# Kernel optimization log

Measured on AMD Instinct MI355X. Metric: run time of the kernel, lower is better.

The kernel has to match this reference:

```python
import jax, jax.numpy as jnp
import numpy as np

B, C_IN, C_OUT, H, W, K = 64, 64, 128, 64, 64, 3


def setup_inputs() -> dict:
    key = jax.random.key(0)
    k1, k2, k3 = jax.random.split(key, 3)
    x = jax.random.normal(k1, (B, C_IN, H, W), dtype=jnp.float32)
    weight = jax.random.normal(k2, (C_OUT, C_IN, K, K), dtype=jnp.float32)
    bias = jax.random.normal(k3, (C_OUT, 1, 1), dtype=jnp.float32)
    return {"x": x, "weight": weight, "bias": bias}


def reference(x, weight, bias):
    # Valid (no pad), stride-1, NCHW direct conv + broadcast bias, matching
    # the naive nested-loop conv2d_multi_in_out + bias of MyConv2D.
    out = jax.lax.conv_general_dilated(
        x, weight,
        window_strides=(1, 1),
        padding="VALID",
        dimension_numbers=("NCHW", "OIHW", "NCHW"),
    )
    return out + bias  # bias (C_out,1,1) broadcasts over (B, C_out, H_out, W_out)
```

## Files before the change

kernel.cpp:

```cpp
#include <hip/hip_runtime.h>

#define CI 64
#define CO 128
#define HH 64
#define WW 64
#define OH 62
#define OW 62

typedef __attribute__((ext_vector_type(8))) short short8x;
typedef __attribute__((ext_vector_type(16))) float f32x16;

__device__ ushort g_wt[9 * CO * CI];

__device__ __forceinline__ ushort bf16rne(float f) {
    unsigned u = __builtin_bit_cast(unsigned, f);
    u += 0x7fffu + ((u >> 16) & 1u);
    return (ushort)(u >> 16);
}

__global__ __launch_bounds__(256)
void wprep(const float* __restrict__ w) {
    const int idx = blockIdx.x * 256 + threadIdx.x;
    const int kk = idx >> 13;
    const int rem = idx & 8191;
    const int co = rem >> 6, ci = rem & 63;
    g_wt[idx] = bf16rne(w[(co * 64 + ci) * 9 + kk]);
}

__global__ __launch_bounds__(256, 2)
void conv_fused(const float* __restrict__ x, const float* __restrict__ bias,
                float* __restrict__ out) {
    __shared__ ushort Xl[264 * 64];
    __shared__ float  sB[CO];

    const int tid = threadIdx.x;
    const int wv = tid >> 6, L = tid & 63, l31 = L & 31, q = L >> 5;
    const int h = wv >> 1;
    const int rw = wv & 1;
    const int b = blockIdx.y, oh0 = blockIdx.x * 2;

    if (tid < CO) sB[tid] = bias[tid];

    const ushort* wbase = g_wt + (h * 64 + l31) * 64 + q * 8;
    short8x wbuf[2][8];
    #pragma unroll
    for (int m = 0; m < 2; ++m)
        #pragma unroll
        for (int s = 0; s < 4; ++s)
            wbuf[0][m * 4 + s] = *(const short8x*)(wbase + m * 2048 + s * 16);

    const float* xb = x + (size_t)b * CI * HH * WW;
    #pragma unroll
    for (int g = 0; g < 2; ++g) {
        const int pxi = tid + g * 256;
        if (g == 0 || tid < 8) {
            const int r = pxi / 66, cpos = pxi - r * 66;
            const bool valid = cpos < 64;
            const float* xcol = xb + (size_t)(oh0 + r) * WW + cpos;
            float vv[64];
            #pragma unroll
            for (int j = 0; j < 64; ++j)
                vv[j] = valid ? xcol[j * (HH * WW)] : 0.f;
            ushort* dst = &Xl[pxi * 64];
            const int pm = pxi & 7;
            #pragma unroll
            for (int c = 0; c < 8; ++c) {
                ushort tmp[8];
                #pragma unroll
                for (int j = 0; j < 8; ++j) tmp[j] = bf16rne(vv[c * 8 + j]);
                *(uint4*)(dst + ((c ^ pm) * 8)) = *(const uint4*)tmp;
            }
        }
    }

    f32x16 acc[2][2];
    #pragma unroll
    for (int i = 0; i < 2; ++i)
        #pragma unroll
        for (int j = 0; j < 2; ++j)
            #pragma unroll
            for (int r = 0; r < 16; ++r) acc[i][j][r] = 0.f;

    __syncthreads();

    #pragma unroll
    for (int kk = 0; kk < 9; ++kk) {
        const short8x* wf = wbuf[kk & 1];
        if (kk < 8) {
            const ushort* nb = wbase + (kk + 1) * (CO * CI);
            #pragma unroll
            for (int m = 0; m < 2; ++m)
                #pragma unroll
                for (int s = 0; s < 4; ++s)
                    wbuf[(kk + 1) & 1][m * 4 + s] = *(const short8x*)(nb + m * 2048 + s * 16);
        }
        const int kr = kk / 3, kc = kk - kr * 3;
        const int pB = (rw + kr) * 66 + kc + l31;
        const ushort* bP0 = Xl + pB * 64;
        const int f0 = pB & 7;
        #pragma unroll
        for (int s = 0; s < 4; ++s) {
            const int ob = (((s * 2 + q) ^ f0) * 8);
            short8x b0 = *(const short8x*)(bP0 + ob);
            short8x b1 = *(const short8x*)(bP0 + 32 * 64 + ob);
            acc[0][0] = __builtin_amdgcn_mfma_f32_32x32x16_bf16(wf[s],     b0, acc[0][0], 0, 0, 0);
            acc[0][1] = __builtin_amdgcn_mfma_f32_32x32x16_bf16(wf[s],     b1, acc[0][1], 0, 0, 0);
            acc[1][0] = __builtin_amdgcn_mfma_f32_32x32x16_bf16(wf[4 + s], b0, acc[1][0], 0, 0, 0);
            acc[1][1] = __builtin_amdgcn_mfma_f32_32x32x16_bf16(wf[4 + s], b1, acc[1][1], 0, 0, 0);
        }
    }

    const int oh = oh0 + rw;
    #pragma unroll
    for (int mt = 0; mt < 2; ++mt)
        #pragma unroll
        for (int nt = 0; nt < 2; ++nt) {
            const int col = nt * 32 + l31;
            if (col < OW) {
                #pragma unroll
                for (int reg = 0; reg < 16; ++reg) {
                    const int co = h * 64 + mt * 32 + 4 * q + (reg & 3) + 8 * (reg >> 2);
                    out[(((size_t)b * CO + co) * OH + oh) * OW + col] = acc[mt][nt][reg] + sB[co];
                }
            }
        }
}

extern "C" void kernel_launch(void* const* d_in, const int* in_sizes, int n_in,
                              void* d_out, int out_size, void* d_ws, size_t ws_size,
                              hipStream_t stream) {
    const float* x    = (const float*)d_in[0];
    const float* wgt  = (const float*)d_in[1];
    const float* bias = (const float*)d_in[2];
    float* out = (float*)d_out;

    wprep<<<dim3(288), 256, 0, stream>>>(wgt);
    conv_fused<<<dim3(31, 64), 256, 0, stream>>>(x, bias, out);
}
```

Baseline: 252.4 us.

## Pre-convert input to channel-last bf16 and stage tiles via direct global-to-LDS loads

Adds an xprep kernel that converts x to bf16 in a channel-innermost, width-padded layout in a global scratch buffer. The conv kernel then fills its LDS tile with global_load_lds 16-byte copies, applying the XOR swizzle on the source address, instead of issuing 64 strided fp32 loads per thread and converting in registers. This is meant to remove per-thread register pressure and load latency from the conv prologue, and launch bounds are raised to allow three blocks per CU. The cost is an extra kernel launch plus a full write and read of the transposed bf16 copy of x.

```diff
diff --git a/kernel.cpp b/kernel.cpp
--- a/kernel.cpp
+++ b/kernel.cpp
@@ -6,16 +6,24 @@
 #define WW 64
 #define OH 62
 #define OW 62
+#define XTW 66
 
 typedef __attribute__((ext_vector_type(8))) short short8x;
 typedef __attribute__((ext_vector_type(16))) float f32x16;
 
-__device__ ushort g_wt[9 * CO * CI];
+__device__ __attribute__((aligned(16))) ushort g_wt[9 * CO * CI];
+__device__ __attribute__((aligned(16))) ushort g_xt[64 * 64 * XTW * 64];
 
 __device__ __forceinline__ ushort bf16rne(float f) {
     unsigned u = __builtin_bit_cast(unsigned, f);
     u += 0x7fffu + ((u >> 16) & 1u);
     return (ushort)(u >> 16);
+}
+
+__device__ __forceinline__ void gld_lds16(const ushort* g, ushort* l) {
+    __builtin_amdgcn_global_load_lds(
+        (const __attribute__((address_space(1))) unsigned*)g,
+        (__attribute__((address_space(3))) unsigned*)l, 16, 0, 0);
 }
 
 __global__ __launch_bounds__(256)
@@ -27,9 +35,43 @@
     g_wt[idx] = bf16rne(w[(co * 64 + ci) * 9 + kk]);
 }
 
-__global__ __launch_bounds__(256, 2)
-void conv_fused(const float* __restrict__ x, const float* __restrict__ bias,
-                float* __restrict__ out) {
+__global__ __launch_bounds__(256)
+void xprep(const float* __restrict__ x) {
+    __shared__ ushort T[64 * 68];
+    const int t = threadIdx.x;
+    const int h = blockIdx.x, b = blockIdx.y;
+    const float* xb = x + ((size_t)b * 64 * 64 + h) * 64;
+
+    #pragma unroll
+    for (int g = 0; g < 4; ++g) {
+        const int ci = g * 16 + (t >> 4);
+        const int w0 = (t & 15) * 4;
+        const float4 v = *(const float4*)(xb + (size_t)ci * 4096 + w0);
+        ushort tmp[4];
+        tmp[0] = bf16rne(v.x); tmp[1] = bf16rne(v.y);
+        tmp[2] = bf16rne(v.z); tmp[3] = bf16rne(v.w);
+        *reinterpret_cast<uint2*>(&T[ci * 68 + w0]) = *reinterpret_cast<const uint2*>(tmp);
+    }
+    __syncthreads();
+
+    ushort* dst = g_xt + (size_t)(b * 64 + h) * XTW * 64;
+    #pragma unroll
+    for (int g = 0; g < 2; ++g) {
+        const int w = g * 32 + (t >> 3);
+        const int cg = t & 7;
+        ushort tmp[8];
+        #pragma unroll
+        for (int j = 0; j < 8; ++j) tmp[j] = T[(cg * 8 + j) * 68 + w];
+        *reinterpret_cast<uint4*>(dst + w * 64 + cg * 8) = *reinterpret_cast<const uint4*>(tmp);
+    }
+    if (t < 16) {
+        const uint4 z{0, 0, 0, 0};
+        *reinterpret_cast<uint4*>(dst + 64 * 64 + t * 8) = z;
+    }
+}
+
+__global__ __launch_bounds__(256, 3)
+void conv_fused(const float* __restrict__ bias, float* __restrict__ out) {
     __shared__ ushort Xl[264 * 64];
     __shared__ float  sB[CO];
 
@@ -49,28 +91,18 @@
         for (int s = 0; s < 4; ++s)
             wbuf[0][m * 4 + s] = *(const short8x*)(wbase + m * 2048 + s * 16);
 
-    const float* xb = x + (size_t)b * CI * HH * WW;
+    const ushort* xTb = g_xt + (size_t)((b * 64 + oh0) * XTW) * 64;
     #pragma unroll
-    for (int g = 0; g < 2; ++g) {
-        const int pxi = tid + g * 256;
-        if (g == 0 || tid < 8) {
-            const int r = pxi / 66, cpos = pxi - r * 66;
-            const bool valid = cpos < 64;
-            const float* xcol = xb + (size_t)(oh0 + r) * WW + cpos;
-            float vv[64];
-            #pragma unroll
-            for (int j = 0; j < 64; ++j)
-                vv[j] = valid ? xcol[j * (HH * WW)] : 0.f;
-            ushort* dst = &Xl[pxi * 64];
-            const int pm = pxi & 7;
-            #pragma unroll
-            for (int c = 0; c < 8; ++c) {
-                ushort tmp[8];
-                #pragma unroll
-                for (int j = 0; j < 8; ++j) tmp[j] = bf16rne(vv[c * 8 + j]);
-                *(uint4*)(dst + ((c ^ pm) * 8)) = *(const uint4*)tmp;
-            }
-        }
+    for (int j = 0; j < 8; ++j) {
+        const int i = j * 256 + tid;
+        const int px = i >> 3, c = i & 7;
+        gld_lds16(xTb + px * 64 + ((c ^ (px & 7)) * 8),
+                  &Xl[(j * 256 + (tid & 192)) * 8]);
+    }
+    if (tid < 64) {
+        const int i = 2048 + tid;
+        const int px = i >> 3, c = i & 7;
+        gld_lds16(xTb + px * 64 + ((c ^ (px & 7)) * 8), &Xl[2048 * 8]);
     }
 
     f32x16 acc[2][2];
@@ -95,7 +127,7 @@
                     wbuf[(kk + 1) & 1][m * 4 + s] = *(const short8x*)(nb + m * 2048 + s * 16);
         }
         const int kr = kk / 3, kc = kk - kr * 3;
-        const int pB = (rw + kr) * 66 + kc + l31;
+        const int pB = (rw + kr) * XTW + kc + l31;
         const ushort* bP0 = Xl + pB * 64;
         const int f0 = pB & 7;
         #pragma unroll
@@ -135,5 +167,6 @@
     float* out = (float*)d_out;
 
     wprep<<<dim3(288), 256, 0, stream>>>(wgt);
-    conv_fused<<<dim3(31, 64), 256, 0, stream>>>(x, bias, out);
+    xprep<<<dim3(64, 64), 256, 0, stream>>>(x);
+    conv_fused<<<dim3(31, 64), 256, 0, stream>>>(bias, out);
 }
```

Result: slower. 273.4 us (+8.4%).
